# Kernel tuning notes

Hardware: AMD Instinct MI355X
Metric: run time of the kernel (lower is better)

## Reference

```python
import jax, jax.numpy as jnp
import numpy as np
from jax import lax

VOCAB = 32000
D = 64
B = 32
S = 512
DECAY_P = 0.1  # p in rho_t = (1-p)*rho_{t-1} + outer(x_t, x_t)


def setup_inputs() -> dict:
    key = jax.random.key(0)
    k1, k2 = jax.random.split(key)
    x = jax.random.randint(k1, (B, S), 0, VOCAB, dtype=jnp.int64)
    emb = jax.random.normal(k2, (VOCAB, D), dtype=jnp.float32)
    return {"x": x, "emb": emb}


def reference(x, emb):
    # Embedding lookup: [B, S, D]
    content = emb[x]
    # Per-token outer products (projectedRho): [B, S, D, D]
    proj = jnp.einsum('bsi,bsj->bsij', content, content)
    # Initial rho = identity, repeated over batch: [B, D, D]
    init_rho = jnp.broadcast_to(jnp.eye(D, dtype=emb.dtype), (B, D, D))
    decay = jnp.asarray(1.0 - DECAY_P, dtype=emb.dtype)

    def step(rho, p_t):
        rho = rho * decay + p_t  # [B, D, D]
        return rho, rho

    # scan over time axis; proj transposed to [S, B, D, D]
    _, states = lax.scan(step, init_rho, jnp.swapaxes(proj, 0, 1))
    # states: [S, B, D, D] -> return as [B, S, D, D] (stacked list of states)
    return jnp.swapaxes(states, 0, 1)
```

## Files before the change

kernel.cpp:

```cpp
#include <hip/hip_runtime.h>

#define VOCAB 32000
#define D     64
#define B     32
#define S     512
#define NCHUNK 8
#define CLEN   64

typedef float vf4 __attribute__((ext_vector_type(4)));

__global__ void qmn_gather(const int* __restrict__ x,
                           const vf4* __restrict__ emb4,
                           vf4* __restrict__ content4) {
    int tid = blockIdx.x * blockDim.x + threadIdx.x;
    int bs  = tid >> 4;
    int d4  = tid & 15;
    int tok = x[bs];
    content4[tid] = emb4[tok * (D / 4) + d4];
}

__global__ __launch_bounds__(256, 4) void qmn_chunks(
    const float* __restrict__ content,
    vf4*        __restrict__ out4)
{
    const float DECAY = 0.9f;

    int blk   = blockIdx.x;
    int c     = blk >> 7;
    int b     = (blk >> 2) & 31;
    int iBase = (blk & 3) * 16;

    int jq = threadIdx.x & 15;
    int i  = iBase + (threadIdx.x >> 4);

    vf4 rho;
    int j0 = jq * 4;
    rho.x = (i == j0 + 0) ? 1.0f : 0.0f;
    rho.y = (i == j0 + 1) ? 1.0f : 0.0f;
    rho.z = (i == j0 + 2) ? 1.0f : 0.0f;
    rho.w = (i == j0 + 3) ? 1.0f : 0.0f;

    const float* cb  = content + (size_t)b * S * D;
    const vf4*   cb4 = (const vf4*)cb;
    const int tStart = c * CLEN;

    #pragma unroll 8
    for (int t = 0; t < tStart; ++t) {
        float ci = cb[t * D + i];
        vf4   cj = cb4[t * (D / 4) + jq];
        rho.x = rho.x * DECAY + ci * cj.x;
        rho.y = rho.y * DECAY + ci * cj.y;
        rho.z = rho.z * DECAY + ci * cj.z;
        rho.w = rho.w * DECAY + ci * cj.w;
    }

    vf4* outp = out4 + (((size_t)(b * S + tStart)) * D + i) * (D / 4) + jq;

    #pragma unroll 4
    for (int tt = 0; tt < CLEN; ++tt) {
        int t = tStart + tt;
        float ci = cb[t * D + i];
        vf4   cj = cb4[t * (D / 4) + jq];
        rho.x = rho.x * DECAY + ci * cj.x;
        rho.y = rho.y * DECAY + ci * cj.y;
        rho.z = rho.z * DECAY + ci * cj.z;
        rho.w = rho.w * DECAY + ci * cj.w;
        *outp = rho;
        outp += D * (D / 4);
    }
}

extern "C" void kernel_launch(void* const* d_in, const int* in_sizes, int n_in,
                              void* d_out, int out_size, void* d_ws, size_t ws_size,
                              hipStream_t stream) {
    const int*   x   = (const int*)d_in[0];
    const float* emb = (const float*)d_in[1];
    vf4* out = (vf4*)d_out;

    float* content = (float*)d_ws;

    qmn_gather<<<B * S * (D / 4) / 256, 256, 0, stream>>>(
        x, (const vf4*)emb, (vf4*)content);

    qmn_chunks<<<B * NCHUNK * 4, 256, 0, stream>>>(content, out);
}
```

Measured before the change: 298.8 us.

## Replace per-chunk prefix recomputation with chunked scan: partials, prefix, then store

```diff
diff --git a/kernel.cpp b/kernel.cpp
--- a/kernel.cpp
+++ b/kernel.cpp
@@ -9,6 +9,9 @@
 
 typedef float vf4 __attribute__((ext_vector_type(4)));
 
+#define DECAY   0.9f
+#define DECAY64 0.0011790184577738602f
+
 __global__ void qmn_gather(const int* __restrict__ x,
                            const vf4* __restrict__ emb4,
                            vf4* __restrict__ content4) {
@@ -19,44 +22,93 @@
     content4[tid] = emb4[tok * (D / 4) + d4];
 }
 
-__global__ __launch_bounds__(256, 4) void qmn_chunks(
+__global__ __launch_bounds__(256, 4) void qmn_partial(
     const float* __restrict__ content,
-    vf4*        __restrict__ out4)
+    vf4*        __restrict__ P4)
 {
-    const float DECAY = 0.9f;
-
     int blk   = blockIdx.x;
-    int c     = blk >> 7;
-    int b     = (blk >> 2) & 31;
     int iBase = (blk & 3) * 16;
+    int c     = (blk >> 2) & 7;
+    int b     = blk >> 5;
 
     int jq = threadIdx.x & 15;
     int i  = iBase + (threadIdx.x >> 4);
 
-    vf4 rho;
+    const float* cb  = content + (size_t)b * S * D;
+    const vf4*   cb4 = (const vf4*)cb;
+    const int    t0  = c * CLEN;
+
+    vf4 acc; acc.x = 0.f; acc.y = 0.f; acc.z = 0.f; acc.w = 0.f;
+
+    #pragma unroll 8
+    for (int tt = 0; tt < CLEN; ++tt) {
+        int t = t0 + tt;
+        float ci = cb[t * D + i];
+        vf4   cj = cb4[t * (D / 4) + jq];
+        acc.x = acc.x * DECAY + ci * cj.x;
+        acc.y = acc.y * DECAY + ci * cj.y;
+        acc.z = acc.z * DECAY + ci * cj.z;
+        acc.w = acc.w * DECAY + ci * cj.w;
+    }
+
+    P4[(((b * NCHUNK + c) * D) + i) * (D / 4) + jq] = acc;
+}
+
+__global__ __launch_bounds__(256) void qmn_prefix(
+    const vf4* __restrict__ P4,
+    vf4*       __restrict__ R4)
+{
+    int tid = blockIdx.x * 256 + threadIdx.x;
+    int jq  = tid & 15;
+    int i   = (tid >> 4) & 63;
+    int b   = tid >> 10;
+
+    vf4 r;
     int j0 = jq * 4;
-    rho.x = (i == j0 + 0) ? 1.0f : 0.0f;
-    rho.y = (i == j0 + 1) ? 1.0f : 0.0f;
-    rho.z = (i == j0 + 2) ? 1.0f : 0.0f;
-    rho.w = (i == j0 + 3) ? 1.0f : 0.0f;
+    r.x = (i == j0 + 0) ? 1.0f : 0.0f;
+    r.y = (i == j0 + 1) ? 1.0f : 0.0f;
+    r.z = (i == j0 + 2) ? 1.0f : 0.0f;
+    r.w = (i == j0 + 3) ? 1.0f : 0.0f;
+
+    const vf4* Pb  = P4 + (size_t)b * NCHUNK * D * (D / 4);
+    vf4*       Rb  = R4 + (size_t)b * NCHUNK * D * (D / 4);
+    const int  off = i * (D / 4) + jq;
+
+    Rb[off] = r;
+
+    #pragma unroll
+    for (int c = 1; c < NCHUNK; ++c) {
+        vf4 p = Pb[(c - 1) * D * (D / 4) + off];
+        r.x = r.x * DECAY64 + p.x;
+        r.y = r.y * DECAY64 + p.y;
+        r.z = r.z * DECAY64 + p.z;
+        r.w = r.w * DECAY64 + p.w;
+        Rb[c * D * (D / 4) + off] = r;
+    }
+}
+
+__global__ __launch_bounds__(256, 4) void qmn_store(
+    const float* __restrict__ content,
+    const vf4*  __restrict__ R4,
+    vf4*        __restrict__ out4)
+{
+    int blk   = blockIdx.x;
+    int iBase = (blk & 3) * 16;
+    int c     = (blk >> 2) & 7;
+    int b     = blk >> 5;
+
+    int jq = threadIdx.x & 15;
+    int i  = iBase + (threadIdx.x >> 4);
+
+    vf4 rho = R4[(((b * NCHUNK + c) * D) + i) * (D / 4) + jq];
 
     const float* cb  = content + (size_t)b * S * D;
     const vf4*   cb4 = (const vf4*)cb;
     const int tStart = c * CLEN;
 
-    #pragma unroll 8
-    for (int t = 0; t < tStart; ++t) {
-        float ci = cb[t * D + i];
-        vf4   cj = cb4[t * (D / 4) + jq];
-        rho.x = rho.x * DECAY + ci * cj.x;
-        rho.y = rho.y * DECAY + ci * cj.y;
-        rho.z = rho.z * DECAY + ci * cj.z;
-        rho.w = rho.w * DECAY + ci * cj.w;
-    }
-
     vf4* outp = out4 + (((size_t)(b * S + tStart)) * D + i) * (D / 4) + jq;
 
-    #pragma unroll 4
+    #pragma unroll 8
     for (int tt = 0; tt < CLEN; ++tt) {
         int t = tStart + tt;
         float ci = cb[t * D + i];
@@ -78,9 +130,15 @@
     vf4* out = (vf4*)d_out;
 
     float* content = (float*)d_ws;
+    vf4*   P4      = (vf4*)((char*)d_ws + (size_t)B * S * D * sizeof(float));
+    vf4*   R4      = (vf4*)((char*)d_ws + 2 * (size_t)B * S * D * sizeof(float));
 
     qmn_gather<<<B * S * (D / 4) / 256, 256, 0, stream>>>(
         x, (const vf4*)emb, (vf4*)content);
 
-    qmn_chunks<<<B * NCHUNK * 4, 256, 0, stream>>>(content, out);
+    qmn_partial<<<B * NCHUNK * 4, 256, 0, stream>>>(content, P4);
+
+    qmn_prefix<<<(B * D * 16) / 256, 256, 0, stream>>>(P4, R4);
+
+    qmn_store<<<B * NCHUNK * 4, 256, 0, stream>>>(content, R4, out);
 }
```

After: 295.8 us. About the same (-1.0%).
